# Optimization experiments

Hardware: AMD Instinct MI355X
Metric: run time of the kernel (lower is better)

Reference implementation:

```python
import jax, jax.numpy as jnp
import numpy as np

L = 32   # latent_dim == enc_dim
ND = 1   # node feature dim (single node type)
B, N = 8, 256
M = 3 * L           # message / Encoder output dim = 2*latent + enc = 96
DIN = 2 * (ND + L) + L  # Encoder input dim = 2*node + 2*latent + enc = 98


def _glorot(key, shape):
    fan_in, fan_out = shape
    s = jnp.sqrt(6.0 / (fan_in + fan_out))
    return jax.random.uniform(key, shape, jnp.float32, -s, s)


def setup_inputs() -> dict:
    key = jax.random.key(0)
    ks = jax.random.split(key, 14)
    return {
        "xs": jax.random.normal(ks[0], (B, N, ND), jnp.float32),
        "hs": jax.random.normal(ks[1], (B, N, L), jnp.float32),
        "e_feat": jax.random.normal(ks[2], (B, N, N, 1), jnp.float32),
        "adj": jax.random.randint(ks[3], (B, N, N), 0, 2, jnp.int32),
        "W_e": _glorot(ks[4], (1, L)),          # edge encoder
        "W_enc_lin": _glorot(ks[5], (DIN, M)),  # Encoder linear branch
        "W_enc_1": _glorot(ks[6], (DIN, M)),    # Encoder non-linear branch
        "W_enc_2": _glorot(ks[7], (M, M)),
        "W_proc_u": _glorot(ks[8], (M, L)),     # processor update
        "W_dec": _glorot(ks[9], (ND + 2 * L, ND)),
        "W_pred": _glorot(ks[10], (2 * L + L, 1)),
        "W_tm": _glorot(ks[11], (2 * L + L, L)),  # termination MPNN message
        "W_tu": _glorot(ks[12], (L, L)),          # termination MPNN update
        "W_term": _glorot(ks[13], (L, 1)),
    }


def reference(xs, hs, adj, e_feat, W_e, W_enc_lin, W_enc_1, W_enc_2,
              W_proc_u, W_dec, W_pred, W_tm, W_tu, W_term):
    b, n = adj.shape[0], adj.shape[1]
    adj2 = adj + jnp.eye(n, dtype=adj.dtype)[None]          # add self-loops
    mask = (adj2 > 0)[..., None]                            # [B,N,N,1]
    neg = jnp.float32(-jnp.inf)

    z = jnp.concatenate([xs, hs], axis=-1)                  # [B,N,ND+L]
    enc_e = jnp.einsum('bije,eh->bijh', e_feat, W_e)        # [B,N,N,L]

    zi = jnp.broadcast_to(z[:, :, None, :], (b, n, n, z.shape[-1]))
    zj = jnp.broadcast_to(z[:, None, :, :], (b, n, n, z.shape[-1]))
    u = jnp.concatenate([zi, zj, enc_e], axis=-1)           # [B,N,N,98]
    # Encoder: linear + 2-layer ReLU MLP (message function)
    msg = u @ W_enc_lin + jax.nn.relu(u @ W_enc_1) @ W_enc_2  # [B,N,N,96]
    agg = jnp.max(jnp.where(mask, msg, neg), axis=2)        # masked max over j
    new_h = agg @ W_proc_u                                  # [B,N,L]

    new_x = jnp.concatenate([z, new_h], axis=-1) @ W_dec    # decoder

    hi = jnp.broadcast_to(new_h[:, :, None, :], (b, n, n, L))
    hj = jnp.broadcast_to(new_h[:, None, :, :], (b, n, n, L))
    hij = jnp.concatenate([hi, hj, enc_e], axis=-1)         # [B,N,N,96]
    p = jnp.where(mask, hij @ W_pred, neg)                  # [B,N,N,1]

    # termination MPNN (tau_in == new_h for single node type)
    mt = jax.nn.relu(hij @ W_tm)                            # [B,N,N,L]
    tau_node = jnp.max(jnp.where(mask, mt, neg), axis=2) @ W_tu
    tau = jnp.mean(tau_node, axis=1) @ W_term               # [B,1]

    cat_h = new_h
    return new_x, p, tau, cat_h
```

## Files before the change

### kernel.cpp

```cpp
#include <hip/hip_runtime.h>
#include <hip/hip_bf16.h>
#include <math.h>

#define BB 8
#define NN 256
#define LLAT 32
#define MM 96
#define ZD 33
#define ROWS (BB*NN)

#define OFF_ALIN   0
#define OFF_BLIN   (OFF_ALIN + ROWS*MM)
#define OFF_A1     (OFF_BLIN + ROWS*MM)
#define OFF_B1     (OFF_A1   + ROWS*MM)
#define OFF_AGG    (OFF_B1   + ROWS*MM)
#define OFF_Z      (OFF_AGG  + ROWS*MM)
#define OFF_NEWH   (OFF_Z    + ROWS*ZD)
#define OFF_PI     (OFF_NEWH + ROWS*LLAT)
#define OFF_PJ     (OFF_PI   + ROWS)
#define OFF_TI     (OFF_PJ   + ROWS)
#define OFF_TJ     (OFF_TI   + ROWS*LLAT)
#define OFF_TAUM   (OFF_TJ   + ROWS*LLAT)
#define OFF_CONST  (OFF_TAUM + ROWS*LLAT)
#define C_LIN   0
#define C_1     96
#define C_PRED  192
#define C_TM    193
#define C_WCOMB 225
#define OFF_W2TH (OFF_CONST + 512)
#define OFF_W2TL (OFF_W2TH + 4992)

#define OUT_NEWX 0
#define OUT_P    2048
#define OUT_TAU  526336
#define OUT_CATH 526344

#define NEG_BIG (-3.0e38f)

typedef __attribute__((ext_vector_type(8))) short bf16x8;
typedef __attribute__((ext_vector_type(4))) float f32x4;

__device__ inline void bf16split(float v, ushort& hi, ushort& lo) {
  __hip_bfloat16 h = __float2bfloat16(v);
  float hf = __bfloat162float(h);
  __hip_bfloat16 l = __float2bfloat16(v - hf);
  hi = *reinterpret_cast<ushort*>(&h);
  lo = *reinterpret_cast<ushort*>(&l);
}

__global__ __launch_bounds__(128) void k_prep(
    const float* __restrict__ xs, const float* __restrict__ hs,
    const float* __restrict__ W_enc_lin, const float* __restrict__ W_enc_1,
    const float* __restrict__ W_e, const float* __restrict__ W_pred,
    const float* __restrict__ W_tm, const float* __restrict__ W_tu,
    const float* __restrict__ W_term, const float* __restrict__ W_enc_2,
    float* __restrict__ ws) {
  int r = blockIdx.x;
  int t = threadIdx.x;
  __shared__ float z[ZD];
  if (t == 0) z[0] = xs[r];
  else if (t < ZD) z[t] = hs[r * LLAT + (t - 1)];
  __syncthreads();
  if (t < ZD) ws[OFF_Z + r * ZD + t] = z[t];
  if (t < 96) {
    float al = 0.f, bl = 0.f, a1 = 0.f, b1 = 0.f;
    #pragma unroll
    for (int k = 0; k < ZD; ++k) {
      float zk = z[k];
      al = fmaf(zk, W_enc_lin[k * 96 + t], al);
      bl = fmaf(zk, W_enc_lin[(ZD + k) * 96 + t], bl);
      a1 = fmaf(zk, W_enc_1[k * 96 + t], a1);
      b1 = fmaf(zk, W_enc_1[(ZD + k) * 96 + t], b1);
    }
    ws[OFF_ALIN + r * 96 + t] = al;
    ws[OFF_BLIN + r * 96 + t] = bl;
    ws[OFF_A1 + r * 96 + t] = a1;
    ws[OFF_B1 + r * 96 + t] = b1;
  }
  if (r < 96) {
    ushort* w2h = (ushort*)(ws + OFF_W2TH);
    ushort* w2l = (ushort*)(ws + OFF_W2TL);
    if (t < 96) {
      ushort hi, lo;
      bf16split(W_enc_2[t * 96 + r], hi, lo);
      w2h[r * 104 + t] = hi;
      w2l[r * 104 + t] = lo;
    }
  } else if (r == 96) {
    float* cst = ws + OFF_CONST;
    if (t < 96) {
      float s0 = 0.f, s1 = 0.f;
      for (int k = 0; k < 32; ++k) {
        float we = W_e[k];
        s0 = fmaf(we, W_enc_lin[(66 + k) * 96 + t], s0);
        s1 = fmaf(we, W_enc_1[(66 + k) * 96 + t], s1);
      }
      cst[C_LIN + t] = s0;
      cst[C_1 + t] = s1;
    }
  } else if (r == 97) {
    float* cst = ws + OFF_CONST;
    if (t < 32) {
      float s_tm = 0.f;
      for (int k = 0; k < 32; ++k) s_tm = fmaf(W_e[k], W_tm[(64 + k) * 32 + t], s_tm);
      cst[C_TM + t] = s_tm;
      float s_wc = 0.f;
      for (int q = 0; q < 32; ++q) s_wc = fmaf(W_tu[t * 32 + q], W_term[q], s_wc);
      cst[C_WCOMB + t] = s_wc;
    } else if (t == 32) {
      float s = 0.f;
      for (int k = 0; k < 32; ++k) s = fmaf(W_e[k], W_pred[64 + k], s);
      cst[C_PRED] = s;
    }
  }
}

__global__ __launch_bounds__(256, 2) void k_main(
    const float* __restrict__ e_feat, const int* __restrict__ adj,
    const float* __restrict__ W_proc_u, const float* __restrict__ W_dec,
    const float* __restrict__ W_pred, const float* __restrict__ W_tm,
    float* __restrict__ ws, float* __restrict__ out) {
  const int bi = blockIdx.x;
  const int i = bi & 255;
  const int brow = bi & ~255;
  const int t = threadIdx.x;
  const int lane = t & 63, wid = t >> 6;
  const int wj = wid >> 1, wc = wid & 1;
  const int l15 = lane & 15, lg = lane >> 4;

  __shared__ __align__(16) ushort W2Ts[2 * 96 * 104];
  __shared__ __align__(16) ushort Vhi[64 * 104];
  __shared__ __align__(16) ushort Vlo[64 * 104];
  __shared__ float A1i[96], ALi[96], c1s[96], cls[96];
  __shared__ float red[4][48];
  __shared__ float aggs[96], nh[32];

  {
    const uint4* src = (const uint4*)(ws + OFF_W2TH);
    uint4* dst = (uint4*)W2Ts;
    for (int idx = t; idx < (2 * 96 * 104) / 8; idx += 256) dst[idx] = src[idx];
  }
  if (t < 96) {
    A1i[t] = ws[OFF_A1 + bi * 96 + t];
    ALi[t] = ws[OFF_ALIN + bi * 96 + t];
    c1s[t] = ws[OFF_CONST + C_1 + t];
    cls[t] = ws[OFF_CONST + C_LIN + t];
  }
  __syncthreads();

  float aliC[3], clsC[3];
  #pragma unroll
  for (int ct = 0; ct < 3; ++ct) {
    const int c = wc * 48 + ct * 16 + l15;
    aliC[ct] = ALi[c];
    clsC[ct] = cls[c];
  }

  const int jl = t & 63, kg = t >> 6;
  const int k0 = kg * 24;

  float rmax[3] = {-INFINITY, -INFINITY, -INFINITY};

  for (int jt = 0; jt < 4; ++jt) {
    const int j0 = jt * 64;
    {
      const int j = j0 + jl;
      const float ej = e_feat[bi * 256 + j];
      const float4* B14 = (const float4*)(ws + OFF_B1 + (brow + j) * 96 + k0);
      #pragma unroll
      for (int q = 0; q < 3; ++q) {
        float4 b0 = B14[2 * q], b1 = B14[2 * q + 1];
        float vv[8] = {b0.x, b0.y, b0.z, b0.w, b1.x, b1.y, b1.z, b1.w};
        bf16x8 h8, l8;
        #pragma unroll
        for (int e = 0; e < 8; ++e) {
          const int k = k0 + q * 8 + e;
          float v = fmaxf(fmaf(ej, c1s[k], A1i[k] + vv[e]), 0.f);
          ushort hi, lo;
          bf16split(v, hi, lo);
          h8[e] = (short)hi;
          l8[e] = (short)lo;
        }
        *(bf16x8*)&Vhi[jl * 104 + k0 + q * 8] = h8;
        *(bf16x8*)&Vlo[jl * 104 + k0 + q * 8] = l8;
      }
    }
    __syncthreads();

    float blp[2][4][3];
    int adjv[2][4];
    float ejv[2][4];
    #pragma unroll
    for (int jg = 0; jg < 2; ++jg) {
      #pragma unroll
      for (int r = 0; r < 4; ++r) {
        const int j = j0 + wj * 32 + jg * 16 + lg * 4 + r;
        adjv[jg][r] = adj[bi * 256 + j];
        ejv[jg][r] = e_feat[bi * 256 + j];
        const float* BLrow = ws + OFF_BLIN + (brow + j) * 96;
        #pragma unroll
        for (int ct = 0; ct < 3; ++ct)
          blp[jg][r][ct] = BLrow[wc * 48 + ct * 16 + l15];
      }
    }

    f32x4 acc[2][3];
    #pragma unroll
    for (int jg = 0; jg < 2; ++jg)
      #pragma unroll
      for (int ct = 0; ct < 3; ++ct) acc[jg][ct] = 0;

    #pragma unroll
    for (int ks = 0; ks < 3; ++ks) {
      const int ka = ks * 32 + lg * 8;
      bf16x8 bh[3], bl[3];
      #pragma unroll
      for (int ct = 0; ct < 3; ++ct) {
        const int br = (wc * 48 + ct * 16 + l15) * 104 + ka;
        bh[ct] = *(const bf16x8*)&W2Ts[br];
        bl[ct] = *(const bf16x8*)&W2Ts[96 * 104 + br];
      }
      #pragma unroll
      for (int jg = 0; jg < 2; ++jg) {
        const int arow = (wj * 32 + jg * 16 + l15) * 104 + ka;
        bf16x8 ah = *(const bf16x8*)&Vhi[arow];
        bf16x8 al = *(const bf16x8*)&Vlo[arow];
        #pragma unroll
        for (int ct = 0; ct < 3; ++ct) {
          acc[jg][ct] = __builtin_amdgcn_mfma_f32_16x16x32_bf16(ah, bh[ct], acc[jg][ct], 0, 0, 0);
          acc[jg][ct] = __builtin_amdgcn_mfma_f32_16x16x32_bf16(ah, bl[ct], acc[jg][ct], 0, 0, 0);
          acc[jg][ct] = __builtin_amdgcn_mfma_f32_16x16x32_bf16(al, bh[ct], acc[jg][ct], 0, 0, 0);
        }
      }
    }

    #pragma unroll
    for (int jg = 0; jg < 2; ++jg) {
      #pragma unroll
      for (int r = 0; r < 4; ++r) {
        const int j = j0 + wj * 32 + jg * 16 + lg * 4 + r;
        const bool msk = (adjv[jg][r] > 0) || (j == i);
        if (msk) {
          const float ej = ejv[jg][r];
          #pragma unroll
          for (int ct = 0; ct < 3; ++ct) {
            float val = acc[jg][ct][r] + aliC[ct] + fmaf(clsC[ct], ej, blp[jg][r][ct]);
            rmax[ct] = fmaxf(rmax[ct], val);
          }
        }
      }
    }
    __syncthreads();
  }

  #pragma unroll
  for (int ct = 0; ct < 3; ++ct) {
    float v = rmax[ct];
    v = fmaxf(v, __shfl_xor(v, 16));
    v = fmaxf(v, __shfl_xor(v, 32));
    rmax[ct] = v;
  }
  if (lane < 16) {
    #pragma unroll
    for (int ct = 0; ct < 3; ++ct) red[wid][ct * 16 + lane] = rmax[ct];
  }
  __syncthreads();
  if (t < 96) {
    const int wcq = t / 48, cc = t % 48;
    aggs[t] = fmaxf(red[wcq][cc], red[wcq + 2][cc]);
  }
  __syncthreads();

  if (t < 32) {
    float s = 0.f;
    #pragma unroll 8
    for (int c = 0; c < 96; ++c) s = fmaf(aggs[c], W_proc_u[c * 32 + t], s);
    nh[t] = s;
    out[OUT_CATH + bi * 32 + t] = s;
  }
  __syncthreads();
  if (t < 32) {
    float si = 0.f, sj = 0.f;
    #pragma unroll
    for (int m = 0; m < 32; ++m) {
      si = fmaf(nh[m], W_tm[m * 32 + t], si);
      sj = fmaf(nh[m], W_tm[(32 + m) * 32 + t], sj);
    }
    ws[OFF_TI + bi * 32 + t] = si;
    ws[OFF_TJ + bi * 32 + t] = sj;
  } else if (t == 32) {
    float s = 0.f;
    for (int k = 0; k < ZD; ++k) s = fmaf(ws[OFF_Z + bi * ZD + k], W_dec[k], s);
    for (int m = 0; m < 32; ++m) s = fmaf(nh[m], W_dec[ZD + m], s);
    out[OUT_NEWX + bi] = s;
  } else if (t == 33) {
    float s = 0.f;
    for (int m = 0; m < 32; ++m) s = fmaf(nh[m], W_pred[m], s);
    ws[OFF_PI + bi] = s;
  } else if (t == 34) {
    float s = 0.f;
    for (int m = 0; m < 32; ++m) s = fmaf(nh[m], W_pred[32 + m], s);
    ws[OFF_PJ + bi] = s;
  }
  if (bi < 8 && t == 36) out[OUT_TAU + bi] = 0.f;
}

__global__ __launch_bounds__(256) void k_pair(
    const float* __restrict__ e_feat, const int* __restrict__ adj,
    float* __restrict__ ws, float* __restrict__ out) {
  int bi = blockIdx.x;
  int i = bi & 255;
  int brow = bi & ~255;
  int t = threadIdx.x;
  __shared__ float Tis[32], ctms[32], partial[8][32];
  __shared__ float Pis, cpred;
  if (t < 32) {
    Tis[t] = ws[OFF_TI + bi * 32 + t];
    ctms[t] = ws[OFF_CONST + C_TM + t];
  } else if (t == 32) {
    Pis = ws[OFF_PI + bi];
  } else if (t == 33) {
    cpred = ws[OFF_CONST + C_PRED];
  }
  __syncthreads();

  {
    const int j = t;
    float ej = e_feat[bi * 256 + j];
    bool msk = (adj[bi * 256 + j] > 0) || (j == i);
    float pv = msk ? (Pis + ws[OFF_PJ + brow + j] + ej * cpred) : NEG_BIG;
    out[OUT_P + bi * 256 + j] = pv;
  }

  {
    const int k = t & 31, g = t >> 5;
    const float tik = Tis[k], ctk = ctms[k];
    const float* Tj = ws + OFF_TJ + brow * 32;
    float m = -INFINITY;
    #pragma unroll 4
    for (int jj = 0; jj < 32; ++jj) {
      const int j = g * 32 + jj;
      float tjv = Tj[j * 32 + k];
      float ejj = e_feat[bi * 256 + j];
      bool mk = (adj[bi * 256 + j] > 0) || (j == i);
      float val = fmaxf(tik + fmaf(ejj, ctk, tjv), 0.f);
      m = mk ? fmaxf(m, val) : m;
    }
    partial[g][k] = m;
  }
  __syncthreads();
  if (t < 32) {
    float v = partial[0][t];
    #pragma unroll
    for (int g = 1; g < 8; ++g) v = fmaxf(v, partial[g][t]);
    float s = v * ws[OFF_CONST + C_WCOMB + t];
    s += __shfl_xor(s, 1);
    s += __shfl_xor(s, 2);
    s += __shfl_xor(s, 4);
    s += __shfl_xor(s, 8);
    s += __shfl_xor(s, 16);
    if (t == 0) atomicAdd(&out[OUT_TAU + (bi >> 8)], s * (1.0f / 256.0f));
  }
}

extern "C" void kernel_launch(void* const* d_in, const int* in_sizes, int n_in,
                              void* d_out, int out_size, void* d_ws, size_t ws_size,
                              hipStream_t stream) {
  const float* xs        = (const float*)d_in[0];
  const float* hs        = (const float*)d_in[1];
  const float* e_feat    = (const float*)d_in[2];
  const int*   adj       = (const int*)d_in[3];
  const float* W_e       = (const float*)d_in[4];
  const float* W_enc_lin = (const float*)d_in[5];
  const float* W_enc_1   = (const float*)d_in[6];
  const float* W_enc_2   = (const float*)d_in[7];
  const float* W_proc_u  = (const float*)d_in[8];
  const float* W_dec     = (const float*)d_in[9];
  const float* W_pred    = (const float*)d_in[10];
  const float* W_tm      = (const float*)d_in[11];
  const float* W_tu      = (const float*)d_in[12];
  const float* W_term    = (const float*)d_in[13];

  float* ws  = (float*)d_ws;
  float* out = (float*)d_out;

  k_prep<<<ROWS, 128, 0, stream>>>(xs, hs, W_enc_lin, W_enc_1, W_e, W_pred,
                                   W_tm, W_tu, W_term, W_enc_2, ws);
  k_main<<<ROWS, 256, 0, stream>>>(e_feat, adj, W_proc_u, W_dec, W_pred, W_tm,
                                   ws, out);
  k_pair<<<ROWS, 256, 0, stream>>>(e_feat, adj, ws, out);
}
```

Measured before the change: 203.4 us.

## Build MFMA A-operands in registers and cover all j with 8 waves

The main kernel now launches 512 threads, and each of the 8 waves owns 32 j-rows and all 96 output columns. Before, 4 waves looped over 4 j-tiles. Each wave computes the ReLU'd split-bf16 A fragments straight from global B1 into registers, so the LDS staging buffers Vhi/Vlo and the per-tile barriers go away. This is meant to cut LDS traffic and synchronisation and to raise parallelism per block. The cost is more accumulator registers per thread and a higher occupancy target in launch bounds, which may force register spills.

```diff
diff --git a/kernel.cpp b/kernel.cpp
--- a/kernel.cpp
+++ b/kernel.cpp
@@ -115,7 +115,7 @@
   }
 }
 
-__global__ __launch_bounds__(256, 2) void k_main(
+__global__ __launch_bounds__(512, 4) void k_main(
     const float* __restrict__ e_feat, const int* __restrict__ adj,
     const float* __restrict__ W_proc_u, const float* __restrict__ W_dec,
     const float* __restrict__ W_pred, const float* __restrict__ W_tm,
@@ -124,21 +124,18 @@
   const int i = bi & 255;
   const int brow = bi & ~255;
   const int t = threadIdx.x;
-  const int lane = t & 63, wid = t >> 6;
-  const int wj = wid >> 1, wc = wid & 1;
+  const int lane = t & 63, w = t >> 6;
   const int l15 = lane & 15, lg = lane >> 4;
 
   __shared__ __align__(16) ushort W2Ts[2 * 96 * 104];
-  __shared__ __align__(16) ushort Vhi[64 * 104];
-  __shared__ __align__(16) ushort Vlo[64 * 104];
   __shared__ float A1i[96], ALi[96], c1s[96], cls[96];
-  __shared__ float red[4][48];
+  __shared__ float red[8][96];
   __shared__ float aggs[96], nh[32];
 
   {
     const uint4* src = (const uint4*)(ws + OFF_W2TH);
     uint4* dst = (uint4*)W2Ts;
-    for (int idx = t; idx < (2 * 96 * 104) / 8; idx += 256) dst[idx] = src[idx];
+    for (int idx = t; idx < 2496; idx += 512) dst[idx] = src[idx];
   }
   if (t < 96) {
     A1i[t] = ws[OFF_A1 + bi * 96 + t];
@@ -148,126 +145,104 @@
   }
   __syncthreads();
 
-  float aliC[3], clsC[3];
-  #pragma unroll
-  for (int ct = 0; ct < 3; ++ct) {
-    const int c = wc * 48 + ct * 16 + l15;
+  float ejA[2];
+  ejA[0] = e_feat[bi * 256 + w * 32 + l15];
+  ejA[1] = e_feat[bi * 256 + w * 32 + 16 + l15];
+
+  f32x4 acc[2][6];
+  #pragma unroll
+  for (int jg = 0; jg < 2; ++jg)
+    #pragma unroll
+    for (int ct = 0; ct < 6; ++ct) acc[jg][ct] = 0;
+
+  #pragma unroll
+  for (int ks = 0; ks < 3; ++ks) {
+    const int ka = ks * 32 + lg * 8;
+    const float4 c1a = *(const float4*)&c1s[ka];
+    const float4 c1b = *(const float4*)&c1s[ka + 4];
+    const float4 a1a = *(const float4*)&A1i[ka];
+    const float4 a1b = *(const float4*)&A1i[ka + 4];
+    const float cc[8] = {c1a.x, c1a.y, c1a.z, c1a.w, c1b.x, c1b.y, c1b.z, c1b.w};
+    const float aa[8] = {a1a.x, a1a.y, a1a.z, a1a.w, a1b.x, a1b.y, a1b.z, a1b.w};
+
+    bf16x8 ah[2], al[2];
+    #pragma unroll
+    for (int jg = 0; jg < 2; ++jg) {
+      const int jr = w * 32 + jg * 16 + l15;
+      const float4* bp = (const float4*)(ws + OFF_B1 + (brow + jr) * 96 + ka);
+      const float4 b0 = bp[0], b1 = bp[1];
+      const float vvv[8] = {b0.x, b0.y, b0.z, b0.w, b1.x, b1.y, b1.z, b1.w};
+      bf16x8 h8, l8;
+      #pragma unroll
+      for (int e = 0; e < 8; ++e) {
+        float v = fmaxf(fmaf(ejA[jg], cc[e], aa[e] + vvv[e]), 0.f);
+        ushort hi, lo;
+        bf16split(v, hi, lo);
+        h8[e] = (short)hi;
+        l8[e] = (short)lo;
+      }
+      ah[jg] = h8;
+      al[jg] = l8;
+    }
+
+    #pragma unroll
+    for (int ct = 0; ct < 6; ++ct) {
+      const int br = (ct * 16 + l15) * 104 + ka;
+      const bf16x8 bh = *(const bf16x8*)&W2Ts[br];
+      const bf16x8 bl = *(const bf16x8*)&W2Ts[96 * 104 + br];
+      #pragma unroll
+      for (int jg = 0; jg < 2; ++jg) {
+        acc[jg][ct] = __builtin_amdgcn_mfma_f32_16x16x32_bf16(ah[jg], bh, acc[jg][ct], 0, 0, 0);
+        acc[jg][ct] = __builtin_amdgcn_mfma_f32_16x16x32_bf16(ah[jg], bl, acc[jg][ct], 0, 0, 0);
+        acc[jg][ct] = __builtin_amdgcn_mfma_f32_16x16x32_bf16(al[jg], bh, acc[jg][ct], 0, 0, 0);
+      }
+    }
+  }
+
+  float aliC[6], clsC[6];
+  #pragma unroll
+  for (int ct = 0; ct < 6; ++ct) {
+    const int c = ct * 16 + l15;
     aliC[ct] = ALi[c];
     clsC[ct] = cls[c];
   }
-
-  const int jl = t & 63, kg = t >> 6;
-  const int k0 = kg * 24;
-
-  float rmax[3] = {-INFINITY, -INFINITY, -INFINITY};
-
-  for (int jt = 0; jt < 4; ++jt) {
-    const int j0 = jt * 64;
-    {
-      const int j = j0 + jl;
+  float rmax[6] = {-INFINITY, -INFINITY, -INFINITY, -INFINITY, -INFINITY, -INFINITY};
+  #pragma unroll
+  for (int jg = 0; jg < 2; ++jg) {
+    #pragma unroll
+    for (int r = 0; r < 4; ++r) {
+      const int j = w * 32 + jg * 16 + lg * 4 + r;
+      const int av = adj[bi * 256 + j];
       const float ej = e_feat[bi * 256 + j];
-      const float4* B14 = (const float4*)(ws + OFF_B1 + (brow + j) * 96 + k0);
-      #pragma unroll
-      for (int q = 0; q < 3; ++q) {
-        float4 b0 = B14[2 * q], b1 = B14[2 * q + 1];
-        float vv[8] = {b0.x, b0.y, b0.z, b0.w, b1.x, b1.y, b1.z, b1.w};
-        bf16x8 h8, l8;
+      const bool msk = (av > 0) || (j == i);
+      if (msk) {
+        const float* BL = ws + OFF_BLIN + (brow + j) * 96;
         #pragma unroll
-        for (int e = 0; e < 8; ++e) {
-          const int k = k0 + q * 8 + e;
-          float v = fmaxf(fmaf(ej, c1s[k], A1i[k] + vv[e]), 0.f);
-          ushort hi, lo;
-          bf16split(v, hi, lo);
-          h8[e] = (short)hi;
-          l8[e] = (short)lo;
-        }
-        *(bf16x8*)&Vhi[jl * 104 + k0 + q * 8] = h8;
-        *(bf16x8*)&Vlo[jl * 104 + k0 + q * 8] = l8;
-      }
-    }
-    __syncthreads();
-
-    float blp[2][4][3];
-    int adjv[2][4];
-    float ejv[2][4];
-    #pragma unroll
-    for (int jg = 0; jg < 2; ++jg) {
-      #pragma unroll
-      for (int r = 0; r < 4; ++r) {
-        const int j = j0 + wj * 32 + jg * 16 + lg * 4 + r;
-        adjv[jg][r] = adj[bi * 256 + j];
-        ejv[jg][r] = e_feat[bi * 256 + j];
-        const float* BLrow = ws + OFF_BLIN + (brow + j) * 96;
-        #pragma unroll
-        for (int ct = 0; ct < 3; ++ct)
-          blp[jg][r][ct] = BLrow[wc * 48 + ct * 16 + l15];
-      }
-    }
-
-    f32x4 acc[2][3];
-    #pragma unroll
-    for (int jg = 0; jg < 2; ++jg)
-      #pragma unroll
-      for (int ct = 0; ct < 3; ++ct) acc[jg][ct] = 0;
-
-    #pragma unroll
-    for (int ks = 0; ks < 3; ++ks) {
-      const int ka = ks * 32 + lg * 8;
-      bf16x8 bh[3], bl[3];
-      #pragma unroll
-      for (int ct = 0; ct < 3; ++ct) {
-        const int br = (wc * 48 + ct * 16 + l15) * 104 + ka;
-        bh[ct] = *(const bf16x8*)&W2Ts[br];
-        bl[ct] = *(const bf16x8*)&W2Ts[96 * 104 + br];
-      }
-      #pragma unroll
-      for (int jg = 0; jg < 2; ++jg) {
-        const int arow = (wj * 32 + jg * 16 + l15) * 104 + ka;
-        bf16x8 ah = *(const bf16x8*)&Vhi[arow];
-        bf16x8 al = *(const bf16x8*)&Vlo[arow];
-        #pragma unroll
-        for (int ct = 0; ct < 3; ++ct) {
-          acc[jg][ct] = __builtin_amdgcn_mfma_f32_16x16x32_bf16(ah, bh[ct], acc[jg][ct], 0, 0, 0);
-          acc[jg][ct] = __builtin_amdgcn_mfma_f32_16x16x32_bf16(ah, bl[ct], acc[jg][ct], 0, 0, 0);
-          acc[jg][ct] = __builtin_amdgcn_mfma_f32_16x16x32_bf16(al, bh[ct], acc[jg][ct], 0, 0, 0);
+        for (int ct = 0; ct < 6; ++ct) {
+          float val = acc[jg][ct][r] + aliC[ct] + fmaf(clsC[ct], ej, BL[ct * 16 + l15]);
+          rmax[ct] = fmaxf(rmax[ct], val);
         }
       }
     }
-
-    #pragma unroll
-    for (int jg = 0; jg < 2; ++jg) {
-      #pragma unroll
-      for (int r = 0; r < 4; ++r) {
-        const int j = j0 + wj * 32 + jg * 16 + lg * 4 + r;
-        const bool msk = (adjv[jg][r] > 0) || (j == i);
-        if (msk) {
-          const float ej = ejv[jg][r];
-          #pragma unroll
-          for (int ct = 0; ct < 3; ++ct) {
-            float val = acc[jg][ct][r] + aliC[ct] + fmaf(clsC[ct], ej, blp[jg][r][ct]);
-            rmax[ct] = fmaxf(rmax[ct], val);
-          }
-        }
-      }
-    }
-    __syncthreads();
-  }
-
-  #pragma unroll
-  for (int ct = 0; ct < 3; ++ct) {
+  }
+
+  #pragma unroll
+  for (int ct = 0; ct < 6; ++ct) {
     float v = rmax[ct];
     v = fmaxf(v, __shfl_xor(v, 16));
     v = fmaxf(v, __shfl_xor(v, 32));
     rmax[ct] = v;
   }
-  if (lane < 16) {
-    #pragma unroll
-    for (int ct = 0; ct < 3; ++ct) red[wid][ct * 16 + lane] = rmax[ct];
+  if (lg == 0) {
+    #pragma unroll
+    for (int ct = 0; ct < 6; ++ct) red[w][ct * 16 + l15] = rmax[ct];
   }
   __syncthreads();
   if (t < 96) {
-    const int wcq = t / 48, cc = t % 48;
-    aggs[t] = fmaxf(red[wcq][cc], red[wcq + 2][cc]);
+    float m = red[0][t];
+    #pragma unroll
+    for (int q = 1; q < 8; ++q) m = fmaxf(m, red[q][t]);
+    aggs[t] = m;
   }
   __syncthreads();
 
@@ -386,7 +361,7 @@
 
   k_prep<<<ROWS, 128, 0, stream>>>(xs, hs, W_enc_lin, W_enc_1, W_e, W_pred,
                                    W_tm, W_tu, W_term, W_enc_2, ws);
-  k_main<<<ROWS, 256, 0, stream>>>(e_feat, adj, W_proc_u, W_dec, W_pred, W_tm,
+  k_main<<<ROWS, 512, 0, stream>>>(e_feat, adj, W_proc_u, W_dec, W_pred, W_tm,
                                    ws, out);
   k_pair<<<ROWS, 256, 0, stream>>>(e_feat, adj, ws, out);
 }
```

New measurement: 188.8 us. -7.2%, faster.
